# Performance work log

Measured on AMD Instinct MI355X. Metric: run time of the kernel, lower is better.

## Reference

```python
import jax, jax.numpy as jnp
import numpy as np

N = 100000   # nodes
E = 800000   # directed edges
IN = 256     # in_channels (== hidden, required by repo's vn MLP dims)
HID = 256    # hidden_channels
OUT = 40     # out_channels (arxiv classes)
EPS = 1e-5


def setup_inputs() -> dict:
    key = jax.random.key(0)
    ks = jax.random.split(key, 8)
    def nrm(k, shape, scale=0.05):
        return jax.random.normal(k, shape, dtype=jnp.float32) * scale
    return {
        "x": nrm(ks[0], (N, IN), 1.0),
        "edge_index": jax.random.randint(ks[1], (2, E), 0, N, dtype=jnp.int32),
        # GCNConv weights (PyG: x @ W, then normalized aggregation, then + bias)
        "W0": nrm(ks[2], (IN, HID)),  "b0": jnp.zeros((HID,), jnp.float32),
        "W1": nrm(ks[3], (HID, HID)), "b1": jnp.zeros((HID,), jnp.float32),
        "W2": nrm(ks[4], (HID, OUT)), "b2": jnp.zeros((OUT,), jnp.float32),
        # BatchNorm1d affine params (batch-stat math, training mode)
        "bn_g0": jnp.ones((HID,), jnp.float32), "bn_b0": jnp.zeros((HID,), jnp.float32),
        "bn_g1": jnp.ones((HID,), jnp.float32), "bn_b1": jnp.zeros((HID,), jnp.float32),
        # virtual node embedding (init to 0 per reset_parameters)
        "vn_emb": jnp.zeros((1, IN), jnp.float32),
        # mlp_vns[0]: Linear(IN,HID) + LayerNorm(HID) + ReLU
        "vn_W0": nrm(ks[5], (IN, HID)),  "vn_b0": jnp.zeros((HID,), jnp.float32),
        "ln_g0": jnp.ones((HID,), jnp.float32), "ln_b0": jnp.zeros((HID,), jnp.float32),
        # mlp_vns[1]: Linear(HID,HID) + LayerNorm(HID) + ReLU
        "vn_W1": nrm(ks[6], (HID, HID)), "vn_b1": jnp.zeros((HID,), jnp.float32),
        "ln_g1": jnp.ones((HID,), jnp.float32), "ln_b1": jnp.zeros((HID,), jnp.float32),
    }


def _forward(x, edge_index, W0, b0, W1, b1, W2, b2, bn_g0, bn_b0, bn_g1, bn_b1,
             vn_emb, vn_W0, vn_b0, ln_g0, ln_b0, vn_W1, vn_b1, ln_g1, ln_b1):
    src, dst = edge_index[0], edge_index[1]
    # GCN symmetric normalization with self-loops: deg = in-degree + 1
    deg = jax.ops.segment_sum(jnp.ones(src.shape, jnp.float32), dst, num_segments=N) + 1.0
    dis = jax.lax.rsqrt(deg)                       # deg^{-1/2}  [N]
    coef = (dis[src] * dis[dst])[:, None]          # edge norm   [E,1]
    self_coef = (dis * dis)[:, None]               # self-loop norm = deg^{-1}  [N,1]

    def gcn(h, W, b):
        h = h @ W                                             # [N, out]
        agg = jax.ops.segment_sum(h[src] * coef, dst, num_segments=N)
        return agg + h * self_coef + b

    def bn(h, g, bv):  # BatchNorm1d, batch statistics over nodes
        mu = h.mean(0)
        var = ((h - mu) ** 2).mean(0)
        return (h - mu) * jax.lax.rsqrt(var + EPS) * g + bv

    def ln(h, g, bv):  # LayerNorm over last dim
        mu = h.mean(-1, keepdims=True)
        var = ((h - mu) ** 2).mean(-1, keepdims=True)
        return (h - mu) * jax.lax.rsqrt(var + EPS) * g + bv

    vx = vn_emb                                   # [1, IN]
    # layer 0
    h = x + vx                                    # virtual-node broadcast
    h = gcn(h, W0, b0)
    h = jax.nn.relu(bn(h, bn_g0, bn_b0))          # dropout = identity (eval)
    pool = jnp.sum(h, axis=0, keepdims=True)      # global_add_pool
    vx = jax.nn.relu(ln((pool + vx) @ vn_W0 + vn_b0, ln_g0, ln_b0))
    # layer 1
    h = h + vx
    h = gcn(h, W1, b1)
    h = jax.nn.relu(bn(h, bn_g1, bn_b1))
    pool = jnp.sum(h, axis=0, keepdims=True)
    vx = jax.nn.relu(ln((pool + vx) @ vn_W1 + vn_b1, ln_g1, ln_b1))
    # layer 2 (output)
    h = h + vx
    h = gcn(h, W2, b2)
    return jax.nn.log_softmax(h, axis=-1)


def reference(x, edge_index, W0, b0, W1, b1, W2, b2, bn_g0, bn_b0, bn_g1, bn_b1,
              vn_emb, vn_W0, vn_b0, ln_g0, ln_b0, vn_W1, vn_b1, ln_g1, ln_b1):
    return _forward(x, edge_index, W0, b0, W1, b1, W2, b2, bn_g0, bn_b0, bn_g1, bn_b1,
                    vn_emb, vn_W0, vn_b0, ln_g0, ln_b0, vn_W1, vn_b1, ln_g1, ln_b1)
```

## Files before the change

### kernel.cpp

```cpp
#include <hip/hip_runtime.h>
#include <hip/hip_bf16.h>
#include <cstdint>

#define N_NODES 100000
#define N_EDGES 800000
#define CH      256
#define COUT    40
#define COUTP   48
#define EPS     1e-5f
#define SCAN_CHUNK 1024
#define NSCAN_BLK  98
#define AGG_NPW 16
#define AGG_BLOCKS 2048
#define AGG_WAVES  (AGG_BLOCKS * 4)

typedef unsigned short u16;
typedef unsigned int   u32;
typedef short s16x8 __attribute__((ext_vector_type(8)));
typedef float f32x4 __attribute__((ext_vector_type(4)));

__device__ __forceinline__ float b2f(u32 u) { return __uint_as_float(u << 16); }
__device__ __forceinline__ u16 f2b(float f) {
    u32 u = __float_as_uint(f);
    u32 r = (u + 0x7fffu + ((u >> 16) & 1u)) >> 16;
    return (u16)r;
}
__device__ __forceinline__ u32 packb(float a, float b) {
    return (u32)f2b(a) | ((u32)f2b(b) << 16);
}
__device__ __forceinline__ void unpack8(uint4 v, float* f) {
    f[0] = b2f(v.x & 0xffffu); f[1] = b2f(v.x >> 16);
    f[2] = b2f(v.y & 0xffffu); f[3] = b2f(v.y >> 16);
    f[4] = b2f(v.z & 0xffffu); f[5] = b2f(v.z >> 16);
    f[6] = b2f(v.w & 0xffffu); f[7] = b2f(v.w >> 16);
}

__global__ void k_count(const int* __restrict__ dst, int* __restrict__ counts) {
    int e = blockIdx.x * 256 + threadIdx.x;
    if (e < N_EDGES) atomicAdd(&counts[dst[e]], 1);
}

__global__ void k_scan1(const int* __restrict__ counts, int* __restrict__ partial,
                        int* __restrict__ blocksums) {
    __shared__ int sdata[256];
    int base = blockIdx.x * SCAN_CHUNK;
    int t = threadIdx.x;
    int v[4]; int s = 0;
    for (int j = 0; j < 4; j++) {
        int i = base + t * 4 + j;
        v[j] = (i < N_NODES) ? counts[i] : 0;
        s += v[j];
    }
    sdata[t] = s; __syncthreads();
    for (int off = 1; off < 256; off <<= 1) {
        int x = (t >= off) ? sdata[t - off] : 0;
        __syncthreads();
        sdata[t] += x;
        __syncthreads();
    }
    int incl = sdata[t];
    int run = incl - s;
    if (t == 255) blocksums[blockIdx.x] = incl;
    for (int j = 0; j < 4; j++) {
        int i = base + t * 4 + j;
        if (i < N_NODES) partial[i] = run;
        run += v[j];
    }
}

__global__ void k_scan3(int* __restrict__ row_start, const int* __restrict__ blocksums,
                        int* __restrict__ cursor, const int* __restrict__ counts,
                        float* __restrict__ dis) {
    __shared__ int sd[128], raw[128];
    int t = threadIdx.x;
    if (t < 128) {
        int v = (t < NSCAN_BLK) ? blocksums[t] : 0;
        sd[t] = v; raw[t] = v;
    }
    __syncthreads();
    for (int off = 1; off < 128; off <<= 1) {
        int x = (t < 128 && t >= off) ? sd[t - off] : 0;
        __syncthreads();
        if (t < 128) sd[t] += x;
        __syncthreads();
    }
    int i = blockIdx.x * 256 + t;
    if (i < N_NODES) {
        int j = i >> 10;
        int v = row_start[i] + (sd[j] - raw[j]);
        row_start[i] = v;
        cursor[i] = v;
        dis[i] = rsqrtf(1.0f + (float)counts[i]);
    }
}

__global__ void k_fill(const int* __restrict__ src, const int* __restrict__ dst,
                       int* __restrict__ cursor, int2* __restrict__ edata,
                       const float* __restrict__ dis) {
    int e = blockIdx.x * 256 + threadIdx.x;
    if (e < N_EDGES) {
        int d = dst[e], s = src[e];
        int p = atomicAdd(&cursor[d], 1);
        int2 v; v.x = s; v.y = __float_as_int(dis[s] * dis[d]);
        edata[p] = v;
    }
}

#define PREP_ZBASE (513 + COUTP)
#define PREP_ZN    (N_NODES + 2560 + 2560)
#define PREP_BLOCKS (PREP_ZBASE + (PREP_ZN + 255) / 256)
__global__ void k_prep(const float* __restrict__ W0, const float* __restrict__ W1,
                       const float* __restrict__ W2,
                       u16* __restrict__ T0, u16* __restrict__ T1, u16* __restrict__ T2,
                       const float* __restrict__ vec, float* __restrict__ v20,
                       int* __restrict__ counts, float* __restrict__ statsA,
                       float* __restrict__ statsB) {
    __shared__ float s[256];
    int b = blockIdx.x, t = threadIdx.x;
    if (b < 256) {
        T0[b * 256 + t] = f2b(W0[t * 256 + b]);
    } else if (b < 512) {
        int n = b - 256;
        T1[n * 256 + t] = f2b(W1[t * 256 + n]);
    } else if (b < 512 + COUTP) {
        int n = b - 512;
        T2[n * 256 + t] = f2b(n < COUT ? W2[t * COUT + n] : 0.f);
    } else if (b == 512 + COUTP) {
        s[t] = vec[t];
        __syncthreads();
        float acc = 0.f;
        for (int k = 0; k < 256; k++) acc += s[k] * W0[k * 256 + t];
        v20[t] = acc;
    } else {
        int idx = (b - PREP_ZBASE) * 256 + t;
        if (idx < N_NODES) counts[idx] = 0;
        else if ((idx -= N_NODES) < 2560) statsA[idx] = 0.f;
        else if ((idx -= 2560) < 2560) statsB[idx] = 0.f;
    }
}

__global__ __launch_bounds__(512) void k_gemm_f32a(const float* __restrict__ A,
                                                   const u16* __restrict__ Wt,
                                                   u16* __restrict__ Hout) {
    __shared__ u16 Bs[256 * 72];
    __shared__ u16 As[128 * 72];
    const int t = threadIdx.x;
    const int wave = t >> 6, lane = t & 63;
    const int lm = lane & 15, quad = lane >> 4;
    const int wr = wave & 1, wc = wave >> 1;
    const int m0 = blockIdx.x * 128;
    const int ar = t >> 2, as_ = (t & 3) * 16;
    const int arow = m0 + ar;
    const int brow = t >> 1, bo = (t & 1) * 32;
    const f32x4 vz = {0.f, 0.f, 0.f, 0.f};
    f32x4 acc[4][4];
    for (int m = 0; m < 4; m++)
        for (int c = 0; c < 4; c++) acc[m][c] = vz;

    for (int k0 = 0; k0 < 256; k0 += 64) {
        {
            const uint4* bsrc = (const uint4*)(Wt + brow * 256 + k0 + bo);
            uint4* bdst = (uint4*)(Bs + brow * 72 + bo);
#pragma unroll
            for (int j = 0; j < 4; j++) bdst[j] = bsrc[j];
            uint4 p0 = {0,0,0,0}, p1 = {0,0,0,0};
            if (arow < N_NODES) {
                const float4* asrc = (const float4*)(A + (size_t)arow * 256 + k0 + as_);
                float4 x0 = asrc[0], x1 = asrc[1], x2 = asrc[2], x3 = asrc[3];
                p0.x = packb(x0.x, x0.y); p0.y = packb(x0.z, x0.w);
                p0.z = packb(x1.x, x1.y); p0.w = packb(x1.z, x1.w);
                p1.x = packb(x2.x, x2.y); p1.y = packb(x2.z, x2.w);
                p1.z = packb(x3.x, x3.y); p1.w = packb(x3.z, x3.w);
            }
            uint4* adst = (uint4*)(As + ar * 72 + as_);
            adst[0] = p0; adst[1] = p1;
        }
        __syncthreads();
#pragma unroll
        for (int kk = 0; kk < 64; kk += 32) {
            s16x8 af[4], bf[4];
#pragma unroll
            for (int m = 0; m < 4; m++)
                af[m] = *(const s16x8*)(As + (wr * 64 + m * 16 + lm) * 72 + kk + quad * 8);
#pragma unroll
            for (int c = 0; c < 4; c++)
                bf[c] = *(const s16x8*)(Bs + (wc * 64 + c * 16 + lm) * 72 + kk + quad * 8);
#pragma unroll
            for (int c = 0; c < 4; c++)
#pragma unroll
                for (int m = 0; m < 4; m++)
                    acc[m][c] = __builtin_amdgcn_mfma_f32_16x16x32_bf16(af[m], bf[c], acc[m][c], 0, 0, 0);
        }
        __syncthreads();
    }
#pragma unroll
    for (int m = 0; m < 4; m++) {
#pragma unroll
        for (int c = 0; c < 4; c++) {
            int col = wc * 64 + c * 16 + lm;
#pragma unroll
            for (int i = 0; i < 4; i++) {
                int row = m0 + wr * 64 + m * 16 + quad * 4 + i;
                if (row < N_NODES) Hout[(size_t)row * 256 + col] = f2b(acc[m][c][i]);
            }
        }
    }
}

__global__ __launch_bounds__(512) void k_gemm_bn(const u16* __restrict__ A,
                                                 const float* __restrict__ stats,
                                                 const float* __restrict__ g,
                                                 const float* __restrict__ bv,
                                                 const u16* __restrict__ Wt,
                                                 u16* __restrict__ Hout,
                                                 float* __restrict__ pool) {
    __shared__ u16 Bs[256 * 72];
    __shared__ u16 As[128 * 72];
    __shared__ float ggs[256], bcs[256], pls[256];
    const int t = threadIdx.x;
    const int wave = t >> 6, lane = t & 63;
    const int lm = lane & 15, quad = lane >> 4;
    const int wr = wave & 1, wc = wave >> 1;
    const int m0 = blockIdx.x * 128;
    const int ar = t >> 2, as_ = (t & 3) * 16;
    const int arow = m0 + ar;
    const int brow = t >> 1, bo = (t & 1) * 32;
    if (t < 256) {
        const float inv = 1.0f / (float)N_NODES;
        float mu = stats[t] * inv;
        float var = stats[256 + t] * inv - mu * mu;
        float rs = rsqrtf(var + EPS);
        float gg = g[t] * rs;
        ggs[t] = gg; bcs[t] = bv[t] - mu * gg;
        pls[t] = 0.f;
    }
    __syncthreads();
    const f32x4 vz = {0.f, 0.f, 0.f, 0.f};
    f32x4 acc[4][4];
    for (int m = 0; m < 4; m++)
        for (int c = 0; c < 4; c++) acc[m][c] = vz;

    for (int k0 = 0; k0 < 256; k0 += 64) {
        {
            const uint4* bsrc = (const uint4*)(Wt + brow * 256 + k0 + bo);
            uint4* bdst = (uint4*)(Bs + brow * 72 + bo);
#pragma unroll
            for (int j = 0; j < 4; j++) bdst[j] = bsrc[j];
            float f[16];
            if (arow < N_NODES) {
                const uint4* asrc = (const uint4*)(A + (size_t)arow * 256 + k0 + as_);
                uint4 r0 = asrc[0], r1 = asrc[1];
                unpack8(r0, f); unpack8(r1, f + 8);
#pragma unroll
                for (int j = 0; j < 16; j++) {
                    int c = k0 + as_ + j;
                    f[j] = fmaxf(f[j] * ggs[c] + bcs[c], 0.f);
                }
            } else {
#pragma unroll
                for (int j = 0; j < 16; j++) f[j] = 0.f;
            }
#pragma unroll
            for (int j = 0; j < 16; j++) {
                float v = f[j];
                v += __shfl_xor(v, 4);  v += __shfl_xor(v, 8);
                v += __shfl_xor(v, 16); v += __shfl_xor(v, 32);
                if (lane < 4) atomicAdd(&pls[k0 + lane * 16 + j], v);
            }
            uint4 p0, p1;
            p0.x = packb(f[0], f[1]);   p0.y = packb(f[2], f[3]);
            p0.z = packb(f[4], f[5]);   p0.w = packb(f[6], f[7]);
            p1.x = packb(f[8], f[9]);   p1.y = packb(f[10], f[11]);
            p1.z = packb(f[12], f[13]); p1.w = packb(f[14], f[15]);
            uint4* adst = (uint4*)(As + ar * 72 + as_);
            adst[0] = p0; adst[1] = p1;
        }
        __syncthreads();
#pragma unroll
        for (int kk = 0; kk < 64; kk += 32) {
            s16x8 af[4], bf[4];
#pragma unroll
            for (int m = 0; m < 4; m++)
                af[m] = *(const s16x8*)(As + (wr * 64 + m * 16 + lm) * 72 + kk + quad * 8);
#pragma unroll
            for (int c = 0; c < 4; c++)
                bf[c] = *(const s16x8*)(Bs + (wc * 64 + c * 16 + lm) * 72 + kk + quad * 8);
#pragma unroll
            for (int c = 0; c < 4; c++)
#pragma unroll
                for (int m = 0; m < 4; m++)
                    acc[m][c] = __builtin_amdgcn_mfma_f32_16x16x32_bf16(af[m], bf[c], acc[m][c], 0, 0, 0);
        }
        __syncthreads();
    }
    if (t < 256) atomicAdd(&pool[(blockIdx.x & 7) * 256 + t], pls[t]);
#pragma unroll
    for (int m = 0; m < 4; m++) {
#pragma unroll
        for (int c = 0; c < 4; c++) {
            int col = wc * 64 + c * 16 + lm;
#pragma unroll
            for (int i = 0; i < 4; i++) {
                int row = m0 + wr * 64 + m * 16 + quad * 4 + i;
                if (row < N_NODES) Hout[(size_t)row * 256 + col] = f2b(acc[m][c][i]);
            }
        }
    }
}

__global__ __launch_bounds__(512) void k_gemm2_bn(const u16* __restrict__ A,
                                                  const float* __restrict__ stats,
                                                  const float* __restrict__ g,
                                                  const float* __restrict__ bv,
                                                  const u16* __restrict__ Wt,
                                                  u16* __restrict__ Hout,
                                                  float* __restrict__ pool) {
    __shared__ u16 Bs[48 * 72];
    __shared__ u16 As[128 * 72];
    __shared__ float ggs[256], bcs[256], pls[256];
    const int t = threadIdx.x;
    const int wave = t >> 6, lane = t & 63;
    const int lm = lane & 15, quad = lane >> 4;
    const int m0 = blockIdx.x * 128;
    const int ar = t >> 2, as_ = (t & 3) * 16;
    const int arow = m0 + ar;
    if (t < 256) {
        const float inv = 1.0f / (float)N_NODES;
        float mu = stats[t] * inv;
        float var = stats[256 + t] * inv - mu * mu;
        float rs = rsqrtf(var + EPS);
        float gg = g[t] * rs;
        ggs[t] = gg; bcs[t] = bv[t] - mu * gg;
        pls[t] = 0.f;
    }
    __syncthreads();
    const f32x4 vz = {0.f, 0.f, 0.f, 0.f};
    f32x4 acc[3]; acc[0] = vz; acc[1] = vz; acc[2] = vz;

    for (int k0 = 0; k0 < 256; k0 += 64) {
        {
            if (t < 48) {
                const uint4* bsrc = (const uint4*)(Wt + t * 256 + k0);
                uint4* bdst = (uint4*)(Bs + t * 72);
#pragma unroll
                for (int j = 0; j < 8; j++) bdst[j] = bsrc[j];
            }
            float f[16];
            if (arow < N_NODES) {
                const uint4* asrc = (const uint4*)(A + (size_t)arow * 256 + k0 + as_);
                uint4 r0 = asrc[0], r1 = asrc[1];
                unpack8(r0, f); unpack8(r1, f + 8);
#pragma unroll
                for (int j = 0; j < 16; j++) {
                    int c = k0 + as_ + j;
                    f[j] = fmaxf(f[j] * ggs[c] + bcs[c], 0.f);
                }
            } else {
#pragma unroll
                for (int j = 0; j < 16; j++) f[j] = 0.f;
            }
#pragma unroll
            for (int j = 0; j < 16; j++) {
                float v = f[j];
                v += __shfl_xor(v, 4);  v += __shfl_xor(v, 8);
                v += __shfl_xor(v, 16); v += __shfl_xor(v, 32);
                if (lane < 4) atomicAdd(&pls[k0 + lane * 16 + j], v);
            }
            uint4 p0, p1;
            p0.x = packb(f[0], f[1]);   p0.y = packb(f[2], f[3]);
            p0.z = packb(f[4], f[5]);   p0.w = packb(f[6], f[7]);
            p1.x = packb(f[8], f[9]);   p1.y = packb(f[10], f[11]);
            p1.z = packb(f[12], f[13]); p1.w = packb(f[14], f[15]);
            uint4* adst = (uint4*)(As + ar * 72 + as_);
            adst[0] = p0; adst[1] = p1;
        }
        __syncthreads();
#pragma unroll
        for (int kk = 0; kk < 64; kk += 32) {
            s16x8 af = *(const s16x8*)(As + (wave * 16 + lm) * 72 + kk + quad * 8);
#pragma unroll
            for (int c = 0; c < 3; c++) {
                s16x8 bf = *(const s16x8*)(Bs + (c * 16 + lm) * 72 + kk + quad * 8);
                acc[c] = __builtin_amdgcn_mfma_f32_16x16x32_bf16(af, bf, acc[c], 0, 0, 0);
            }
        }
        __syncthreads();
    }
    if (t < 256) atomicAdd(&pool[(blockIdx.x & 7) * 256 + t], pls[t]);
#pragma unroll
    for (int c = 0; c < 3; c++) {
        int col = c * 16 + lm;
#pragma unroll
        for (int i = 0; i < 4; i++) {
            int row = m0 + wave * 16 + quad * 4 + i;
            if (row < N_NODES) Hout[(size_t)row * COUTP + col] = f2b(acc[c][i]);
        }
    }
}

__global__ __launch_bounds__(256) void k_agg(const u16* __restrict__ H2,
                                             const int* __restrict__ row_start,
                                             const int* __restrict__ counts,
                                             const int2* __restrict__ edata,
                                             const float* __restrict__ dis,
                                             const float* __restrict__ bias,
                                             const float* __restrict__ v2,
                                             u16* __restrict__ OutB,
                                             float* __restrict__ stats) {
    __shared__ float ls[512];
    const int t = threadIdx.x, wave = t >> 6, lane = t & 63;
    const int half = lane >> 5, hl = lane & 31;
    const int ci = hl * 8;
    const float4 bbA = *(const float4*)(bias + ci);
    const float4 bbB = *(const float4*)(bias + ci + 4);
    const float4 vvA = *(const float4*)(v2 + ci);
    const float4 vvB = *(const float4*)(v2 + ci + 4);
    float s[8], q[8];
#pragma unroll
    for (int j = 0; j < 8; j++) { s[j] = 0.f; q[j] = 0.f; }

    const int gwave = blockIdx.x * 4 + wave;
    const int nid = gwave + lane * AGG_WAVES;
    const bool nv = (lane < AGG_NPW) && (nid < N_NODES);
    const int   my_rs = nv ? row_start[nid] : 0;
    const int   my_ct = nv ? counts[nid] : 0;
    const float my_dn = nv ? dis[nid] : 0.f;

    int beg = __shfl(my_rs, 0), cnt = __shfl(my_ct, 0);
    int2 my_e = {0, 0};
    if (lane < cnt) my_e = edata[beg + lane];

    for (int i = 0; i < AGG_NPW; i++) {
        const int node = gwave + i * AGG_WAVES;
        if (node >= N_NODES) break;
        const int2 cur_e = my_e;
        const int  ccnt = cnt, cbeg = beg;
        const float dn = __shfl(my_dn, i);
        const uint4 rs_ = *(const uint4*)(H2 + (size_t)node * 256 + ci);
        if (i + 1 < AGG_NPW && node + AGG_WAVES < N_NODES) {
            beg = __shfl(my_rs, i + 1);
            cnt = __shfl(my_ct, i + 1);
            int2 tmp = {0, 0};
            if (lane < cnt) tmp = edata[beg + lane];
            my_e = tmp;
        }
        const int cnt64 = ccnt < 64 ? ccnt : 64;
        const int cnt8 = (cnt64 + 7) & ~7;
        float a[8];
#pragma unroll
        for (int j = 0; j < 8; j++) a[j] = 0.f;
        float cs = 0.f;
        for (int e = 0; e < cnt8; e += 8) {
            const int   si0 = __shfl(cur_e.x, e + half);
            const int   si1 = __shfl(cur_e.x, e + 2 + half);
            const int   si2 = __shfl(cur_e.x, e + 4 + half);
            const int   si3 = __shfl(cur_e.x, e + 6 + half);
            const float cf0 = __int_as_float(__shfl(cur_e.y, e + half));
            const float cf1 = __int_as_float(__shfl(cur_e.y, e + 2 + half));
            const float cf2 = __int_as_float(__shfl(cur_e.y, e + 4 + half));
            const float cf3 = __int_as_float(__shfl(cur_e.y, e + 6 + half));
            const uint4 r0 = *(const uint4*)(H2 + (size_t)si0 * 256 + ci);
            const uint4 r1 = *(const uint4*)(H2 + (size_t)si1 * 256 + ci);
            const uint4 r2 = *(const uint4*)(H2 + (size_t)si2 * 256 + ci);
            const uint4 r3 = *(const uint4*)(H2 + (size_t)si3 * 256 + ci);
            cs += cf0 + cf1 + cf2 + cf3;
            a[0] += cf0*b2f(r0.x&0xffffu) + cf1*b2f(r1.x&0xffffu) + cf2*b2f(r2.x&0xffffu) + cf3*b2f(r3.x&0xffffu);
            a[1] += cf0*b2f(r0.x>>16)     + cf1*b2f(r1.x>>16)     + cf2*b2f(r2.x>>16)     + cf3*b2f(r3.x>>16);
            a[2] += cf0*b2f(r0.y&0xffffu) + cf1*b2f(r1.y&0xffffu) + cf2*b2f(r2.y&0xffffu) + cf3*b2f(r3.y&0xffffu);
            a[3] += cf0*b2f(r0.y>>16)     + cf1*b2f(r1.y>>16)     + cf2*b2f(r2.y>>16)     + cf3*b2f(r3.y>>16);
            a[4] += cf0*b2f(r0.z&0xffffu) + cf1*b2f(r1.z&0xffffu) + cf2*b2f(r2.z&0xffffu) + cf3*b2f(r3.z&0xffffu);
            a[5] += cf0*b2f(r0.z>>16)     + cf1*b2f(r1.z>>16)     + cf2*b2f(r2.z>>16)     + cf3*b2f(r3.z>>16);
            a[6] += cf0*b2f(r0.w&0xffffu) + cf1*b2f(r1.w&0xffffu) + cf2*b2f(r2.w&0xffffu) + cf3*b2f(r3.w&0xffffu);
            a[7] += cf0*b2f(r0.w>>16)     + cf1*b2f(r1.w>>16)     + cf2*b2f(r2.w>>16)     + cf3*b2f(r3.w>>16);
        }
        if (ccnt > 64) {
            int e2 = 64;
            for (; e2 + 2 <= ccnt; e2 += 2) {
                const int2 ed_ = edata[cbeg + e2 + half];
                const float cf = __int_as_float(ed_.y);
                const uint4 r = *(const uint4*)(H2 + (size_t)ed_.x * 256 + ci);
                cs += cf;
                a[0] += cf*b2f(r.x&0xffffu); a[1] += cf*b2f(r.x>>16);
                a[2] += cf*b2f(r.y&0xffffu); a[3] += cf*b2f(r.y>>16);
                a[4] += cf*b2f(r.z&0xffffu); a[5] += cf*b2f(r.z>>16);
                a[6] += cf*b2f(r.w&0xffffu); a[7] += cf*b2f(r.w>>16);
            }
            if (e2 < ccnt && half == 0) {
                const int2 ed_ = edata[cbeg + e2];
                const float cf = __int_as_float(ed_.y);
                const uint4 r = *(const uint4*)(H2 + (size_t)ed_.x * 256 + ci);
                cs += cf;
                a[0] += cf*b2f(r.x&0xffffu); a[1] += cf*b2f(r.x>>16);
                a[2] += cf*b2f(r.y&0xffffu); a[3] += cf*b2f(r.y>>16);
                a[4] += cf*b2f(r.z&0xffffu); a[5] += cf*b2f(r.z>>16);
                a[6] += cf*b2f(r.w&0xffffu); a[7] += cf*b2f(r.w>>16);
            }
        }
        cs += __shfl_xor(cs, 32);
#pragma unroll
        for (int j = 0; j < 8; j++) a[j] += __shfl_xor(a[j], 32);
        const float sc = dn * dn, cv = cs + sc;
        const float f0 = a[0] + sc*b2f(rs_.x&0xffffu) + cv*vvA.x + bbA.x;
        const float f1 = a[1] + sc*b2f(rs_.x>>16)     + cv*vvA.y + bbA.y;
        const float f2 = a[2] + sc*b2f(rs_.y&0xffffu) + cv*vvA.z + bbA.z;
        const float f3 = a[3] + sc*b2f(rs_.y>>16)     + cv*vvA.w + bbA.w;
        const float f4 = a[4] + sc*b2f(rs_.z&0xffffu) + cv*vvB.x + bbB.x;
        const float f5 = a[5] + sc*b2f(rs_.z>>16)     + cv*vvB.y + bbB.y;
        const float f6 = a[6] + sc*b2f(rs_.w&0xffffu) + cv*vvB.z + bbB.z;
        const float f7 = a[7] + sc*b2f(rs_.w>>16)     + cv*vvB.w + bbB.w;
        if (half == 0) {
            uint4 o;
            o.x = packb(f0, f1); o.y = packb(f2, f3);
            o.z = packb(f4, f5); o.w = packb(f6, f7);
            *(uint4*)(OutB + (size_t)node * 256 + ci) = o;
        }
        s[0] += f0; q[0] += f0*f0;  s[1] += f1; q[1] += f1*f1;
        s[2] += f2; q[2] += f2*f2;  s[3] += f3; q[3] += f3*f3;
        s[4] += f4; q[4] += f4*f4;  s[5] += f5; q[5] += f5*f5;
        s[6] += f6; q[6] += f6*f6;  s[7] += f7; q[7] += f7*f7;
    }
    ls[t] = 0.f; ls[256 + t] = 0.f;
    __syncthreads();
    if (half == 0) {
#pragma unroll
        for (int j = 0; j < 8; j++) {
            atomicAdd(&ls[ci + j], s[j]);
            atomicAdd(&ls[256 + ci + j], q[j]);
        }
    }
    __syncthreads();
    atomicAdd(&stats[t], ls[t]);
    atomicAdd(&stats[256 + t], ls[256 + t]);
}

__global__ void k_vx(const float* __restrict__ pool, const float* __restrict__ vx_old,
                     const float* __restrict__ vnW, const float* __restrict__ vnb,
                     const float* __restrict__ lng, const float* __restrict__ lnb,
                     float* __restrict__ vx_new,
                     const float* __restrict__ Wnext, int ncn, int npn,
                     float* __restrict__ v2n) {
    __shared__ float s[256];
    __shared__ float red[256];
    int t = threadIdx.x;
    float pv = 0.f;
#pragma unroll
    for (int r = 0; r < 8; r++) pv += pool[r * 256 + t];
    s[t] = pv + vx_old[t];
    __syncthreads();
    float y = vnb[t];
    for (int k = 0; k < 256; k++) y += s[k] * vnW[k * 256 + t];
    red[t] = y; __syncthreads();
    for (int off = 128; off > 0; off >>= 1) {
        if (t < off) red[t] += red[t + off];
        __syncthreads();
    }
    float mu = red[0] * (1.f / 256.f);
    __syncthreads();
    float d = y - mu;
    red[t] = d * d; __syncthreads();
    for (int off = 128; off > 0; off >>= 1) {
        if (t < off) red[t] += red[t + off];
        __syncthreads();
    }
    float var = red[0] * (1.f / 256.f);
    float v = fmaxf(d * rsqrtf(var + EPS) * lng[t] + lnb[t], 0.f);
    vx_new[t] = v;
    __syncthreads();
    s[t] = v;
    __syncthreads();
    float acc = 0.f;
    if (t < ncn) {
        for (int k = 0; k < 256; k++) acc += s[k] * Wnext[k * ncn + t];
    }
    if (t < npn) v2n[t] = acc;
}

__global__ __launch_bounds__(256) void k_agg2(const u16* __restrict__ H2,
                                              const int* __restrict__ row_start,
                                              const int* __restrict__ counts,
                                              const int2* __restrict__ edata,
                                              const float* __restrict__ dis,
                                              const float* __restrict__ bias,
                                              const float* __restrict__ v2,
                                              float* __restrict__ OutF) {
    const int t = threadIdx.x, wave = t >> 6, lane = t & 63;
    const int half = lane >> 5, hl = lane & 31;
    const bool gact = hl < 24;
    const bool cact = hl < 20;
    const int c0 = 2 * hl;
    float bb0 = 0.f, bb1 = 0.f, vv0 = 0.f, vv1 = 0.f;
    if (cact) {
        float2 bv = *(const float2*)(bias + c0); bb0 = bv.x; bb1 = bv.y;
        float2 vvv = *(const float2*)(v2 + c0);  vv0 = vvv.x; vv1 = vvv.y;
    }
    const int nbase = blockIdx.x * 16 + wave * 4;
    for (int i = 0; i < 4; i++) {
        const int node = nbase + i;
        const int beg = row_start[node], cnt = counts[node];
        const float dn = dis[node];
        float a0 = 0.f, a1 = 0.f, cs = 0.f;
        int e = half;
        for (; e + 6 < cnt; e += 8) {
            int2 ea = edata[beg+e],   eb = edata[beg+e+2];
            int2 ec = edata[beg+e+4], ed = edata[beg+e+6];
            float ca = __int_as_float(ea.y), cb = __int_as_float(eb.y);
            float cc = __int_as_float(ec.y), cd = __int_as_float(ed.y);
            u32 ra = 0, rb = 0, rc = 0, rd = 0;
            if (gact) {
                ra = *(const u32*)(H2 + (size_t)ea.x * COUTP + c0);
                rb = *(const u32*)(H2 + (size_t)eb.x * COUTP + c0);
                rc = *(const u32*)(H2 + (size_t)ec.x * COUTP + c0);
                rd = *(const u32*)(H2 + (size_t)ed.x * COUTP + c0);
            }
            cs += ca + cb + cc + cd;
            a0 += ca*b2f(ra&0xffffu) + cb*b2f(rb&0xffffu) + cc*b2f(rc&0xffffu) + cd*b2f(rd&0xffffu);
            a1 += ca*b2f(ra>>16)     + cb*b2f(rb>>16)     + cc*b2f(rc>>16)     + cd*b2f(rd>>16);
        }
        for (; e < cnt; e += 2) {
            int2 ea = edata[beg+e];
            float ca = __int_as_float(ea.y);
            u32 ra = gact ? *(const u32*)(H2 + (size_t)ea.x * COUTP + c0) : 0u;
            cs += ca;
            a0 += ca*b2f(ra&0xffffu); a1 += ca*b2f(ra>>16);
        }
        a0 += __shfl_xor(a0, 32);
        a1 += __shfl_xor(a1, 32);
        cs += __shfl_xor(cs, 32);
        const float sc = dn * dn;
        u32 rs_ = gact ? *(const u32*)(H2 + (size_t)node * COUTP + c0) : 0u;
        float h0 = a0 + sc*b2f(rs_&0xffffu) + (cs+sc)*vv0 + bb0;
        float h1 = a1 + sc*b2f(rs_>>16)     + (cs+sc)*vv1 + bb1;
        float m = cact ? fmaxf(h0, h1) : -3.0e38f;
#pragma unroll
        for (int off = 16; off > 0; off >>= 1) m = fmaxf(m, __shfl_xor(m, off));
        float ex = cact ? (expf(h0 - m) + expf(h1 - m)) : 0.f;
        float se = ex;
#pragma unroll
        for (int off = 16; off > 0; off >>= 1) se += __shfl_xor(se, off);
        float lg = logf(se);
        if (cact && half == 0) {
            float2 o = {h0 - m - lg, h1 - m - lg};
            *(float2*)(OutF + (size_t)node * COUT + c0) = o;
        }
    }
}

extern "C" void kernel_launch(void* const* d_in, const int* in_sizes, int n_in,
                              void* d_out, int out_size, void* d_ws, size_t ws_size,
                              hipStream_t stream) {
    const float* x   = (const float*)d_in[0];
    const int*   ei  = (const int*)d_in[1];
    const int*   esrc = ei;
    const int*   edst = ei + N_EDGES;
    const float* W0 = (const float*)d_in[2];  const float* b0 = (const float*)d_in[3];
    const float* W1 = (const float*)d_in[4];  const float* b1 = (const float*)d_in[5];
    const float* W2 = (const float*)d_in[6];  const float* b2 = (const float*)d_in[7];
    const float* bg0 = (const float*)d_in[8]; const float* bb0 = (const float*)d_in[9];
    const float* bg1 = (const float*)d_in[10]; const float* bb1 = (const float*)d_in[11];
    const float* vn_emb = (const float*)d_in[12];
    const float* vW0 = (const float*)d_in[13]; const float* vb0 = (const float*)d_in[14];
    const float* lg0 = (const float*)d_in[15]; const float* lb0 = (const float*)d_in[16];
    const float* vW1 = (const float*)d_in[17]; const float* vb1 = (const float*)d_in[18];
    const float* lg1 = (const float*)d_in[19]; const float* lb1 = (const float*)d_in[20];

    char* w = (char*)d_ws;
    auto alloc = [&](size_t bytes) { void* p = (void*)w; w += ((bytes + 255) / 256) * 256; return p; };
    u16* H2    = (u16*)alloc((size_t)N_NODES * 256 * 2);
    u16* OutB  = (u16*)alloc((size_t)N_NODES * 256 * 2);
    int2* edata = (int2*)alloc((size_t)N_EDGES * 8);
    int* counts = (int*)alloc((size_t)N_NODES * 4);
    int* rowst  = (int*)alloc((size_t)N_NODES * 4);
    int* cursor = (int*)alloc((size_t)N_NODES * 4);
    float* dis  = (float*)alloc((size_t)N_NODES * 4);
    u16* Wtb0 = (u16*)alloc(256 * 256 * 2);
    u16* Wtb1 = (u16*)alloc(256 * 256 * 2);
    u16* Wt2b = (u16*)alloc(COUTP * 256 * 2);
    int* scanblk = (int*)alloc(128 * 4);
    float* statsA = (float*)alloc(2560 * 4);
    float* statsB = (float*)alloc(2560 * 4);
    float* vxA = (float*)alloc(256 * 4);
    float* vxB = (float*)alloc(256 * 4);
    float* v20 = (float*)alloc(256 * 4);
    float* v21 = (float*)alloc(256 * 4);
    float* v22 = (float*)alloc(64 * 4);
    (void)ws_size; (void)in_sizes; (void)n_in; (void)out_size;

    k_prep<<<PREP_BLOCKS, 256, 0, stream>>>(W0, W1, W2, Wtb0, Wtb1, Wt2b,
                                            vn_emb, v20, counts, statsA, statsB);
    k_count<<<(N_EDGES + 255) / 256, 256, 0, stream>>>(edst, counts);
    k_scan1<<<NSCAN_BLK, 256, 0, stream>>>(counts, rowst, scanblk);
    k_scan3<<<(N_NODES + 255) / 256, 256, 0, stream>>>(rowst, scanblk, cursor, counts, dis);
    k_fill<<<(N_EDGES + 255) / 256, 256, 0, stream>>>(esrc, edst, cursor, edata, dis);

    const int gemmblk = (N_NODES + 127) / 128;

    k_gemm_f32a<<<gemmblk, 512, 0, stream>>>(x, Wtb0, H2);
    k_agg<<<AGG_BLOCKS, 256, 0, stream>>>(H2, rowst, counts, edata, dis, b0, v20, OutB, statsA);
    k_gemm_bn<<<gemmblk, 512, 0, stream>>>(OutB, statsA, bg0, bb0, Wtb1, H2, statsA + 512);
    k_vx<<<1, 256, 0, stream>>>(statsA + 512, vn_emb, vW0, vb0, lg0, lb0, vxA, W1, 256, 256, v21);
    k_agg<<<AGG_BLOCKS, 256, 0, stream>>>(H2, rowst, counts, edata, dis, b1, v21, OutB, statsB);
    k_gemm2_bn<<<gemmblk, 512, 0, stream>>>(OutB, statsB, bg1, bb1, Wt2b, H2, statsB + 512);
    k_vx<<<1, 256, 0, stream>>>(statsB + 512, vxA, vW1, vb1, lg1, lb1, vxB, W2, COUT, COUTP, v22);
    k_agg2<<<N_NODES / 16, 256, 0, stream>>>(H2, rowst, counts, edata, dis, b2, v22, (float*)d_out);
}
```

Baseline: 719.4 us.

## Prefetch next A tile in GEMMs, pad output width, nontemporal edge stores

Each of the three GEMM kernels now loads the next k-slice of A into registers before computing on the current one, so global load latency overlaps with the LDS writes and MFMA work. The padded output width grows from 48 to 64, which makes final-layer rows 128 bytes and lets the last GEMM use four full MFMA column tiles. The final aggregation only gathers the 40 active columns. The CSR fill writes each edge record with a nontemporal store. The prefetch raises register pressure, and the wider padding adds GEMM work and memory for H2.

```diff
diff --git a/kernel.cpp b/kernel.cpp
--- a/kernel.cpp
+++ b/kernel.cpp
@@ -6,7 +6,7 @@
 #define N_EDGES 800000
 #define CH      256
 #define COUT    40
-#define COUTP   48
+#define COUTP   64
 #define EPS     1e-5f
 #define SCAN_CHUNK 1024
 #define NSCAN_BLK  98
@@ -101,8 +101,9 @@
     if (e < N_EDGES) {
         int d = dst[e], s = src[e];
         int p = atomicAdd(&cursor[d], 1);
-        int2 v; v.x = s; v.y = __float_as_int(dis[s] * dis[d]);
-        edata[p] = v;
+        unsigned long long payload = (unsigned long long)(u32)s |
+            ((unsigned long long)(u32)__float_as_uint(dis[s] * dis[d]) << 32);
+        __builtin_nontemporal_store(payload, (unsigned long long*)&edata[p]);
     }
 }
 
@@ -157,6 +158,12 @@
     for (int m = 0; m < 4; m++)
         for (int c = 0; c < 4; c++) acc[m][c] = vz;
 
+    float4 xa0 = {0,0,0,0}, xa1 = xa0, xa2 = xa0, xa3 = xa0;
+    if (arow < N_NODES) {
+        const float4* asrc = (const float4*)(A + (size_t)arow * 256 + as_);
+        xa0 = asrc[0]; xa1 = asrc[1]; xa2 = asrc[2]; xa3 = asrc[3];
+    }
+
     for (int k0 = 0; k0 < 256; k0 += 64) {
         {
             const uint4* bsrc = (const uint4*)(Wt + brow * 256 + k0 + bo);
@@ -165,15 +172,17 @@
             for (int j = 0; j < 4; j++) bdst[j] = bsrc[j];
             uint4 p0 = {0,0,0,0}, p1 = {0,0,0,0};
             if (arow < N_NODES) {
-                const float4* asrc = (const float4*)(A + (size_t)arow * 256 + k0 + as_);
-                float4 x0 = asrc[0], x1 = asrc[1], x2 = asrc[2], x3 = asrc[3];
-                p0.x = packb(x0.x, x0.y); p0.y = packb(x0.z, x0.w);
-                p0.z = packb(x1.x, x1.y); p0.w = packb(x1.z, x1.w);
-                p1.x = packb(x2.x, x2.y); p1.y = packb(x2.z, x2.w);
-                p1.z = packb(x3.x, x3.y); p1.w = packb(x3.z, x3.w);
+                p0.x = packb(xa0.x, xa0.y); p0.y = packb(xa0.z, xa0.w);
+                p0.z = packb(xa1.x, xa1.y); p0.w = packb(xa1.z, xa1.w);
+                p1.x = packb(xa2.x, xa2.y); p1.y = packb(xa2.z, xa2.w);
+                p1.z = packb(xa3.x, xa3.y); p1.w = packb(xa3.z, xa3.w);
             }
             uint4* adst = (uint4*)(As + ar * 72 + as_);
             adst[0] = p0; adst[1] = p1;
+            if (k0 + 64 < 256 && arow < N_NODES) {
+                const float4* anext = (const float4*)(A + (size_t)arow * 256 + k0 + 64 + as_);
+                xa0 = anext[0]; xa1 = anext[1]; xa2 = anext[2]; xa3 = anext[3];
+            }
         }
         __syncthreads();
 #pragma unroll
@@ -240,6 +249,12 @@
     for (int m = 0; m < 4; m++)
         for (int c = 0; c < 4; c++) acc[m][c] = vz;
 
+    uint4 rA0 = {0,0,0,0}, rA1 = {0,0,0,0};
+    if (arow < N_NODES) {
+        const uint4* asrc = (const uint4*)(A + (size_t)arow * 256 + as_);
+        rA0 = asrc[0]; rA1 = asrc[1];
+    }
+
     for (int k0 = 0; k0 < 256; k0 += 64) {
         {
             const uint4* bsrc = (const uint4*)(Wt + brow * 256 + k0 + bo);
@@ -248,9 +263,7 @@
             for (int j = 0; j < 4; j++) bdst[j] = bsrc[j];
             float f[16];
             if (arow < N_NODES) {
-                const uint4* asrc = (const uint4*)(A + (size_t)arow * 256 + k0 + as_);
-                uint4 r0 = asrc[0], r1 = asrc[1];
-                unpack8(r0, f); unpack8(r1, f + 8);
+                unpack8(rA0, f); unpack8(rA1, f + 8);
 #pragma unroll
                 for (int j = 0; j < 16; j++) {
                     int c = k0 + as_ + j;
@@ -259,6 +272,10 @@
             } else {
 #pragma unroll
                 for (int j = 0; j < 16; j++) f[j] = 0.f;
+            }
+            if (k0 + 64 < 256 && arow < N_NODES) {
+                const uint4* anext = (const uint4*)(A + (size_t)arow * 256 + k0 + 64 + as_);
+                rA0 = anext[0]; rA1 = anext[1];
             }
 #pragma unroll
             for (int j = 0; j < 16; j++) {
@@ -315,7 +332,7 @@
                                                   const u16* __restrict__ Wt,
                                                   u16* __restrict__ Hout,
                                                   float* __restrict__ pool) {
-    __shared__ u16 Bs[48 * 72];
+    __shared__ u16 Bs[COUTP * 72];
     __shared__ u16 As[128 * 72];
     __shared__ float ggs[256], bcs[256], pls[256];
     const int t = threadIdx.x;
@@ -335,11 +352,17 @@
     }
     __syncthreads();
     const f32x4 vz = {0.f, 0.f, 0.f, 0.f};
-    f32x4 acc[3]; acc[0] = vz; acc[1] = vz; acc[2] = vz;
+    f32x4 acc[4]; acc[0] = vz; acc[1] = vz; acc[2] = vz; acc[3] = vz;
+
+    uint4 rA0 = {0,0,0,0}, rA1 = {0,0,0,0};
+    if (arow < N_NODES) {
+        const uint4* asrc = (const uint4*)(A + (size_t)arow * 256 + as_);
+        rA0 = asrc[0]; rA1 = asrc[1];
+    }
 
     for (int k0 = 0; k0 < 256; k0 += 64) {
         {
-            if (t < 48) {
+            if (t < COUTP) {
                 const uint4* bsrc = (const uint4*)(Wt + t * 256 + k0);
                 uint4* bdst = (uint4*)(Bs + t * 72);
 #pragma unroll
@@ -347,9 +370,7 @@
             }
             float f[16];
             if (arow < N_NODES) {
-                const uint4* asrc = (const uint4*)(A + (size_t)arow * 256 + k0 + as_);
-                uint4 r0 = asrc[0], r1 = asrc[1];
-                unpack8(r0, f); unpack8(r1, f + 8);
+                unpack8(rA0, f); unpack8(rA1, f + 8);
 #pragma unroll
                 for (int j = 0; j < 16; j++) {
                     int c = k0 + as_ + j;
@@ -358,6 +379,10 @@
             } else {
 #pragma unroll
                 for (int j = 0; j < 16; j++) f[j] = 0.f;
+            }
+            if (k0 + 64 < 256 && arow < N_NODES) {
+                const uint4* anext = (const uint4*)(A + (size_t)arow * 256 + k0 + 64 + as_);
+                rA0 = anext[0]; rA1 = anext[1];
             }
 #pragma unroll
             for (int j = 0; j < 16; j++) {
@@ -379,7 +404,7 @@
         for (int kk = 0; kk < 64; kk += 32) {
             s16x8 af = *(const s16x8*)(As + (wave * 16 + lm) * 72 + kk + quad * 8);
 #pragma unroll
-            for (int c = 0; c < 3; c++) {
+            for (int c = 0; c < 4; c++) {
                 s16x8 bf = *(const s16x8*)(Bs + (c * 16 + lm) * 72 + kk + quad * 8);
                 acc[c] = __builtin_amdgcn_mfma_f32_16x16x32_bf16(af, bf, acc[c], 0, 0, 0);
             }
@@ -388,7 +413,7 @@
     }
     if (t < 256) atomicAdd(&pool[(blockIdx.x & 7) * 256 + t], pls[t]);
 #pragma unroll
-    for (int c = 0; c < 3; c++) {
+    for (int c = 0; c < 4; c++) {
         int col = c * 16 + lm;
 #pragma unroll
         for (int i = 0; i < 4; i++) {
@@ -585,7 +610,6 @@
                                               float* __restrict__ OutF) {
     const int t = threadIdx.x, wave = t >> 6, lane = t & 63;
     const int half = lane >> 5, hl = lane & 31;
-    const bool gact = hl < 24;
     const bool cact = hl < 20;
     const int c0 = 2 * hl;
     float bb0 = 0.f, bb1 = 0.f, vv0 = 0.f, vv1 = 0.f;
@@ -606,7 +630,7 @@
             float ca = __int_as_float(ea.y), cb = __int_as_float(eb.y);
             float cc = __int_as_float(ec.y), cd = __int_as_float(ed.y);
             u32 ra = 0, rb = 0, rc = 0, rd = 0;
-            if (gact) {
+            if (cact) {
                 ra = *(const u32*)(H2 + (size_t)ea.x * COUTP + c0);
                 rb = *(const u32*)(H2 + (size_t)eb.x * COUTP + c0);
                 rc = *(const u32*)(H2 + (size_t)ec.x * COUTP + c0);
@@ -619,7 +643,7 @@
         for (; e < cnt; e += 2) {
             int2 ea = edata[beg+e];
             float ca = __int_as_float(ea.y);
-            u32 ra = gact ? *(const u32*)(H2 + (size_t)ea.x * COUTP + c0) : 0u;
+            u32 ra = cact ? *(const u32*)(H2 + (size_t)ea.x * COUTP + c0) : 0u;
             cs += ca;
             a0 += ca*b2f(ra&0xffffu); a1 += ca*b2f(ra>>16);
         }
@@ -627,7 +651,7 @@
         a1 += __shfl_xor(a1, 32);
         cs += __shfl_xor(cs, 32);
         const float sc = dn * dn;
-        u32 rs_ = gact ? *(const u32*)(H2 + (size_t)node * COUTP + c0) : 0u;
+        u32 rs_ = cact ? *(const u32*)(H2 + (size_t)node * COUTP + c0) : 0u;
         float h0 = a0 + sc*b2f(rs_&0xffffu) + (cs+sc)*vv0 + bb0;
         float h1 = a1 + sc*b2f(rs_>>16)     + (cs+sc)*vv1 + bb1;
         float m = cact ? fmaxf(h0, h1) : -3.0e38f;
@@ -682,7 +706,7 @@
     float* vxB = (float*)alloc(256 * 4);
     float* v20 = (float*)alloc(256 * 4);
     float* v21 = (float*)alloc(256 * 4);
-    float* v22 = (float*)alloc(64 * 4);
+    float* v22 = (float*)alloc(COUTP * 4);
     (void)ws_size; (void)in_sizes; (void)n_in; (void)out_size;
 
     k_prep<<<PREP_BLOCKS, 256, 0, stream>>>(W0, W1, W2, Wtb0, Wtb1, Wt2b,
```

Result: slower. 738.4 us (+2.6%).
